# Performance work log

Measured on AMD Instinct MI355X. Metric: run time of the kernel, lower is better.

The kernel has to match this reference:

```python
import jax, jax.numpy as jnp
import numpy as np

B, P, D = 256, 128, 768        # batch, property slots per sample, encoder hidden dim
E = 64                          # num_properties (number of adapter heads)
H = 256                         # adapter_hidden_dim
H2 = H // 2
O = 2                           # output_dim
LN_EPS = 1e-5
RES_W_ADPT, RES_W_BASE = 0.7, 0.3


def setup_inputs() -> dict:
    key = jax.random.key(0)
    ks = jax.random.split(key, 12)
    hidden_states = jax.random.normal(ks[0], (B, P, D), dtype=jnp.float32)
    base_output = jax.random.normal(ks[1], (B, P, O), dtype=jnp.float32)
    properties = jax.random.randint(ks[2], (B, P), 0, E, dtype=jnp.int64)
    mask = (jax.random.uniform(ks[3], (B, P)) > 0.1).astype(jnp.float32)
    # Stacked per-head adapter parameters (LayerNorm + 3 Linears per head)
    ln_g = jnp.ones((E, D), dtype=jnp.float32)
    ln_b = jnp.zeros((E, D), dtype=jnp.float32)
    W1 = jax.random.normal(ks[4], (E, D, H), dtype=jnp.float32) * (1.0 / np.sqrt(D))
    b1 = jnp.zeros((E, H), dtype=jnp.float32)
    W2 = jax.random.normal(ks[5], (E, H, H2), dtype=jnp.float32) * (1.0 / np.sqrt(H))
    b2 = jnp.zeros((E, H2), dtype=jnp.float32)
    W3 = jax.random.normal(ks[6], (E, H2, O), dtype=jnp.float32) * 0.01  # init std=0.01 per source
    b3 = jnp.zeros((E, O), dtype=jnp.float32)
    return {
        "hidden_states": hidden_states, "base_output": base_output,
        "properties": properties, "mask": mask,
        "ln_g": ln_g, "ln_b": ln_b, "W1": W1, "b1": b1,
        "W2": W2, "b2": b2, "W3": W3, "b3": b3,
    }


def reference(hidden_states, base_output, properties, mask,
              ln_g, ln_b, W1, b1, W2, b2, W3, b3):
    b, p, d = hidden_states.shape
    o = W3.shape[-1]
    x = hidden_states.reshape(-1, d)                        # [N, D]
    # LayerNorm statistics are head-independent; only gamma/beta differ per head
    mu = jnp.mean(x, axis=-1, keepdims=True)
    var = jnp.mean((x - mu) ** 2, axis=-1, keepdims=True)
    xhat = (x - mu) * jax.lax.rsqrt(var + LN_EPS)           # [N, D]
    flat_p = properties.reshape(-1)                         # [N]
    flat_m = mask.reshape(-1)                               # [N]

    def body(acc, inp):
        idx, g, bt, w1, bb1, w2, bb2, w3, bb3 = inp
        h = jax.nn.relu((xhat * g + bt) @ w1 + bb1)         # [N, H]  (dropout = identity in eval)
        h = jax.nn.relu(h @ w2 + bb2)                       # [N, H2]
        out = h @ w3 + bb3                                  # [N, O]
        sel = (flat_p == idx) & (flat_m > 0)
        return jnp.where(sel[:, None], out, acc), None

    e = W1.shape[0]
    acc0 = jnp.zeros((b * p, o), dtype=x.dtype)
    acc, _ = jax.lax.scan(
        body, acc0,
        (jnp.arange(e), ln_g, ln_b, W1, b1, W2, b2, W3, b3))
    out = acc.reshape(b, p, o)
    out = RES_W_ADPT * out + RES_W_BASE * base_output       # use_residual=True
    return out * mask[..., None]
```

## Files before the change

kernel.cpp:

```cpp
#include <hip/hip_runtime.h>
#include <stdint.h>

typedef unsigned short u16;
typedef unsigned int   u32;

#define NTOK   32768
#define GD     768
#define GH     256
#define GH2    128
#define GE     64

typedef __bf16 bf16x8 __attribute__((ext_vector_type(8)));
typedef float  f32x4  __attribute__((ext_vector_type(4)));
union Frag { uint4 u; bf16x8 b; };

__device__ __forceinline__ float bf2f(u16 h) {
  union { u32 u; float f; } v; v.u = ((u32)h) << 16; return v.f;
}
__device__ __forceinline__ u16 f2bf(float f) {
  union { float f; u32 u; } v; v.f = f;
  u32 r = (v.u + 0x7fffu + ((v.u >> 16) & 1u)) >> 16;
  return (u16)r;
}

__device__ __forceinline__ void async16(void* lds, const void* g) {
  __builtin_amdgcn_global_load_lds(
      (const __attribute__((address_space(1))) void*)g,
      (__attribute__((address_space(3))) void*)lds, 16, 0, 0);
}

__device__ __forceinline__ int getProp(const int* p32, int t, int is64) {
  return is64 ? p32[2 * t] : p32[t];
}

static const size_t OFF_Y    = 0;
static const size_t OFF_W1T  = 50331648;
static const size_t OFF_W2T  = 75497472;
static const size_t OFF_TOK  = 79691776;
static const size_t OFF_META = 79822848;

__global__ void setup_kernel(const int* __restrict__ prop, const float* __restrict__ mask,
                             u32* __restrict__ outz, int* __restrict__ counts2d,
                             int* __restrict__ cursors_p, int* __restrict__ flagp) {
  __shared__ int h[GE];
  __shared__ int vOr;
  const int b = blockIdx.x;
  const int tid = threadIdx.x;
  outz[b * 512 + tid] = 0u;
  outz[b * 512 + 256 + tid] = 0u;
  if (b < 4) cursors_p[b * 256 + tid] = 0;
  if (tid < GE) h[tid] = 0;
  if (tid == 0) vOr = 0;
  __syncthreads();
  int v = prop[2 * tid + 1] | prop[2 * (tid + 256) + 1];
  if (v) atomicOr(&vOr, 1);
  __syncthreads();
  const int is64 = (vOr == 0) ? 1 : 0;
  if (b == 0 && tid == 0) *flagp = is64;
  const int t = b * 256 + tid;
  if (mask[t] > 0.f) atomicAdd(&h[getProp(prop, t, is64)], 1);
  __syncthreads();
  if (tid < GE) counts2d[b * GE + tid] = h[tid];
}

__global__ void transpose_w1(const float* __restrict__ in, u16* __restrict__ out) {
  __shared__ u16 tl[64][260];
  const int bid = blockIdx.x;
  const int e  = bid / 12, r = bid % 12;
  const int d0 = (r / 4) * 256, h0 = (r % 4) * 64;
  const int tid = threadIdx.x;
  const size_t inMat = (size_t)e * GD * GH;
  const size_t outMat = (size_t)e * GH * GD;
  const int h_l = (tid & 15) * 4, d_l = tid >> 4;
#pragma unroll
  for (int dd = 0; dd < 16; ++dd) {
    const int d = d_l + dd * 16;
    float4 v = *(const float4*)(in + inMat + (size_t)(d0 + d) * GH + h0 + h_l);
    tl[h_l + 0][d] = f2bf(v.x);
    tl[h_l + 1][d] = f2bf(v.y);
    tl[h_l + 2][d] = f2bf(v.z);
    tl[h_l + 3][d] = f2bf(v.w);
  }
  __syncthreads();
  const int wv = tid >> 6, ln = tid & 63;
#pragma unroll
  for (int hh = 0; hh < 16; ++hh) {
    const int h = wv * 16 + hh;
    *(uint2*)(out + outMat + (size_t)(h0 + h) * GD + d0 + ln * 4) =
        *(const uint2*)&tl[h][ln * 4];
  }
}

__global__ void transpose_kernel(const float* __restrict__ in, u16* __restrict__ out,
                                 int R, int C, int tilesC) {
  __shared__ u16 tile[32][33];
  const int tilesPerMat = (R >> 5) * tilesC;
  const int e  = blockIdx.x / tilesPerMat;
  const int t  = blockIdx.x % tilesPerMat;
  const int tr = t / tilesC, tc = t % tilesC;
  const size_t mat = (size_t)e * R * C;
  const int tx = threadIdx.x & 31, ty = threadIdx.x >> 5;
  const int r0 = tr * 32, c0 = tc * 32;
#pragma unroll
  for (int i = 0; i < 32; i += 8)
    tile[ty + i][tx] = f2bf(in[mat + (size_t)(r0 + ty + i) * C + c0 + tx]);
  __syncthreads();
#pragma unroll
  for (int i = 0; i < 32; i += 8)
    out[mat + (size_t)(c0 + ty + i) * R + r0 + tx] = tile[tx][ty + i];
}

__global__ void ln_kernel(const float* __restrict__ hs, const float* __restrict__ g,
                          const float* __restrict__ bta, const int* __restrict__ prop,
                          u16* __restrict__ y, const int* __restrict__ flag) {
  const int wv = threadIdx.x >> 6, ln = threadIdx.x & 63;
  const int t = blockIdx.x * 4 + wv;
  const float* x = hs + (size_t)t * GD;
  float v[12];
  float s = 0.f, sq = 0.f;
#pragma unroll
  for (int c = 0; c < 3; ++c) {
    float4 u = *(const float4*)(x + c * 256 + ln * 4);
    v[c*4+0] = u.x; v[c*4+1] = u.y; v[c*4+2] = u.z; v[c*4+3] = u.w;
    s  += u.x + u.y + u.z + u.w;
    sq += u.x*u.x + u.y*u.y + u.z*u.z + u.w*u.w;
  }
#pragma unroll
  for (int d = 1; d < 64; d <<= 1) { s += __shfl_xor(s, d); sq += __shfl_xor(sq, d); }
  const float mu = s * (1.f / 768.f);
  const float rstd = rsqrtf(sq * (1.f / 768.f) - mu * mu + 1e-5f);
  const int p = getProp(prop, t, *flag);
  const float* gp = g + (size_t)p * GD;
  const float* bp = bta + (size_t)p * GD;
  u16* yp = y + (size_t)t * GD;
#pragma unroll
  for (int c = 0; c < 3; ++c) {
    float4 ug = *(const float4*)(gp + c * 256 + ln * 4);
    float4 ub = *(const float4*)(bp + c * 256 + ln * 4);
    float y0 = (v[c*4+0] - mu) * rstd * ug.x + ub.x;
    float y1 = (v[c*4+1] - mu) * rstd * ug.y + ub.y;
    float y2 = (v[c*4+2] - mu) * rstd * ug.z + ub.z;
    float y3 = (v[c*4+3] - mu) * rstd * ug.w + ub.w;
    uint2 o;
    o.x = (u32)f2bf(y0) | ((u32)f2bf(y1) << 16);
    o.y = (u32)f2bf(y2) | ((u32)f2bf(y3) << 16);
    *(uint2*)(yp + c * 256 + ln * 4) = o;
  }
}

__global__ void scan_kernel(const int* __restrict__ counts2d, int* __restrict__ offsets,
                            int* __restrict__ tileHead, int* __restrict__ tileRow,
                            int* __restrict__ nTilesPtr) {
  const int e = threadIdx.x;
  int c = 0;
  for (int b = 0; b < 128; ++b) c += counts2d[b * GE + e];
  int inc = c;
#pragma unroll
  for (int d = 1; d < 64; d <<= 1) { int n = __shfl_up(inc, d); if (e >= d) inc += n; }
  const int off = inc - c;
  offsets[e] = off;
  if (e == 63) offsets[64] = inc;
  int ntile = (c + 63) >> 6;
  int inct = ntile;
#pragma unroll
  for (int d = 1; d < 64; d <<= 1) { int n = __shfl_up(inct, d); if (e >= d) inct += n; }
  const int tb = inct - ntile;
  for (int j = 0; j < ntile; ++j) { tileHead[tb + j] = e; tileRow[tb + j] = off + j * 64; }
  if (e == 63) *nTilesPtr = inct;
}

__global__ void scatter_kernel(const int* __restrict__ prop, const float* __restrict__ mask,
                               const int* __restrict__ offsets, int* __restrict__ cursors_p,
                               int* __restrict__ tokenIds, const int* __restrict__ flag) {
  __shared__ int h[GE];
  __shared__ int basebin[GE];
  const int tid = threadIdx.x;
  const int t = blockIdx.x * 256 + tid;
  if (tid < GE) h[tid] = 0;
  __syncthreads();
  int p = -1, rank = 0;
  if (mask[t] > 0.f) {
    p = getProp(prop, t, *flag);
    rank = atomicAdd(&h[p], 1);
  }
  __syncthreads();
  if (tid < GE && h[tid] > 0) basebin[tid] = atomicAdd(&cursors_p[tid * 16], h[tid]);
  __syncthreads();
  if (p >= 0) tokenIds[offsets[p] + basebin[p] + rank] = t;
}

__global__ __launch_bounds__(256, 2) void adapter_gemm(
    const u16* __restrict__ y, const u16* __restrict__ w1t, const u16* __restrict__ w2t,
    const float* __restrict__ b1, const float* __restrict__ b2,
    const float* __restrict__ w3, const float* __restrict__ b3,
    const float* __restrict__ base, const float* __restrict__ mask,
    const int* __restrict__ tokenIds, const int* __restrict__ offsets,
    const int* __restrict__ tileHead, const int* __restrict__ tileRow,
    const int* __restrict__ nTilesPtr, float* __restrict__ outp) {
  __shared__ union LU {
    struct { u16 A[2][2048]; u16 B[2][8192]; } s;
    u16 h[17408];
  } uni;
  __shared__ u16 sB2[2][4096];
  __shared__ float sBias1[256];
  __shared__ float sBias2[128];
  __shared__ float sW3[2][128];
  __shared__ float sB3[2];
  __shared__ int   sTok[64];

  const int tid  = threadIdx.x;
  const int wv   = tid >> 6;
  const int ln   = tid & 63;
  const int l15  = tid & 15;
  const int quad = (tid & 63) >> 4;
  const f32x4 vzero = {0.f, 0.f, 0.f, 0.f};
  const int nt = *nTilesPtr;

  for (int tile = blockIdx.x; tile < nt; tile += gridDim.x) {
    __syncthreads();
    const int e  = tileHead[tile];
    const int rs = tileRow[tile];
    const int nRows = min(64, offsets[e + 1] - rs);

    if (tid < 64) sTok[tid] = tokenIds[rs + min(tid, nRows - 1)];
    sBias1[tid] = b1[e * GH + tid];
    if (tid < 128) sBias2[tid] = b2[e * GH2 + tid];
    { const int k = tid >> 1, o = tid & 1; sW3[o][k] = w3[e * GH2 * 2 + k * 2 + o]; }
    if (tid < 2) sB3[tid] = b3[e * 2 + tid];
    __syncthreads();

    const u16* yrow = y + (size_t)sTok[ln] * GD;
    const u16* w1e = w1t + (size_t)e * GH * GD;
    const u16* w2e = w2t + (size_t)e * GH2 * GH;

    f32x4 acc1[4][4];
#pragma unroll
    for (int f = 0; f < 4; ++f)
#pragma unroll
      for (int g = 0; g < 4; ++g) acc1[f][g] = vzero;

    {
      async16(uni.s.A[0] + wv * 512, yrow + wv * 8);
#pragma unroll
      for (int j = 0; j < 4; ++j)
        async16(uni.s.B[0] + wv * 2048 + j * 512,
                w1e + (size_t)(j * 64 + ln) * GD + wv * 8);
    }

    for (int kt = 0; kt < 24; ++kt) {
      __syncthreads();
      if (kt + 1 < 24) {
        const int k0 = (kt + 1) * 32;
        const int par = (kt + 1) & 1;
        async16(uni.s.A[par] + wv * 512, yrow + k0 + wv * 8);
#pragma unroll
        for (int j = 0; j < 4; ++j)
          async16(uni.s.B[par] + wv * 2048 + j * 512,
                  w1e + (size_t)(j * 64 + ln) * GD + k0 + wv * 8);
      }
      const int par = kt & 1;
      Frag fa[4], fb[4];
#pragma unroll
      for (int f = 0; f < 4; ++f)
        fa[f].u = *(const uint4*)&uni.s.A[par][quad * 512 + (f * 16 + l15) * 8];
#pragma unroll
      for (int g = 0; g < 4; ++g)
        fb[g].u = *(const uint4*)&uni.s.B[par][quad * 2048 + (wv * 64 + g * 16 + l15) * 8];
#pragma unroll
      for (int f = 0; f < 4; ++f)
#pragma unroll
        for (int g = 0; g < 4; ++g)
          acc1[f][g] = __builtin_amdgcn_mfma_f32_16x16x32_bf16(fa[f].b, fb[g].b, acc1[f][g], 0, 0, 0);
    }
    __syncthreads();

#pragma unroll
    for (int j = 0; j < 2; ++j)
      async16(sB2[0] + wv * 1024 + j * 512,
              w2e + (size_t)(j * 64 + ln) * GH + wv * 8);

#pragma unroll
    for (int f = 0; f < 4; ++f)
#pragma unroll
      for (int g = 0; g < 4; ++g) {
        const int col = wv * 64 + g * 16 + l15;
        const float bias = sBias1[col];
#pragma unroll
        for (int r = 0; r < 4; ++r) {
          const int row = f * 16 + quad * 4 + r;
          uni.h[row * 264 + col] = f2bf(fmaxf(acc1[f][g][r] + bias, 0.f));
        }
      }

    f32x4 acc2[4][2];
#pragma unroll
    for (int f = 0; f < 4; ++f)
#pragma unroll
      for (int g = 0; g < 2; ++g) acc2[f][g] = vzero;

    for (int kt = 0; kt < 8; ++kt) {
      __syncthreads();
      if (kt + 1 < 8) {
        const int k0 = (kt + 1) * 32;
        const int par = (kt + 1) & 1;
#pragma unroll
        for (int j = 0; j < 2; ++j)
          async16(sB2[par] + wv * 1024 + j * 512,
                  w2e + (size_t)(j * 64 + ln) * GH + k0 + wv * 8);
      }
      const int par = kt & 1;
      Frag fa2[4], fb2[2];
#pragma unroll
      for (int f = 0; f < 4; ++f)
        fa2[f].u = *(const uint4*)&uni.h[(f * 16 + l15) * 264 + kt * 32 + quad * 8];
#pragma unroll
      for (int g = 0; g < 2; ++g)
        fb2[g].u = *(const uint4*)&sB2[par][quad * 1024 + (wv * 32 + g * 16 + l15) * 8];
#pragma unroll
      for (int f = 0; f < 4; ++f)
#pragma unroll
        for (int g = 0; g < 2; ++g)
          acc2[f][g] = __builtin_amdgcn_mfma_f32_16x16x32_bf16(fa2[f].b, fb2[g].b, acc2[f][g], 0, 0, 0);
    }
    __syncthreads();

#pragma unroll
    for (int f = 0; f < 4; ++f)
#pragma unroll
      for (int g = 0; g < 2; ++g) {
        const int col = wv * 32 + g * 16 + l15;
        const float bias = sBias2[col];
#pragma unroll
        for (int r = 0; r < 4; ++r) {
          const int row = f * 16 + quad * 4 + r;
          uni.h[row * 130 + col] = f2bf(fmaxf(acc2[f][g][r] + bias, 0.f));
        }
      }
    __syncthreads();

    const int m = tid >> 1, o = tid & 1;
    if (m < nRows) {
      float a = sB3[o];
      const u16* h2row = &uni.h[m * 130];
#pragma unroll 16
      for (int k = 0; k < 128; ++k) a += bf2f(h2row[k]) * sW3[o][k];
      const int t = sTok[m];
      const float mk = mask[t];
      const float bs = base[t * 2 + o];
      outp[t * 2 + o] = (0.7f * a + 0.3f * bs) * mk;
    }
  }
}

extern "C" void kernel_launch(void* const* d_in, const int* in_sizes, int n_in,
                              void* d_out, int out_size, void* d_ws, size_t ws_size,
                              hipStream_t stream) {
  const float* hs   = (const float*)d_in[0];
  const float* base = (const float*)d_in[1];
  const int*   prop = (const int*)d_in[2];
  const float* mask = (const float*)d_in[3];
  const float* lng  = (const float*)d_in[4];
  const float* lnb  = (const float*)d_in[5];
  const float* W1   = (const float*)d_in[6];
  const float* b1   = (const float*)d_in[7];
  const float* W2   = (const float*)d_in[8];
  const float* b2   = (const float*)d_in[9];
  const float* W3   = (const float*)d_in[10];
  const float* b3   = (const float*)d_in[11];

  char* ws = (char*)d_ws;
  u16* y    = (u16*)(ws + OFF_Y);
  u16* w1t  = (u16*)(ws + OFF_W1T);
  u16* w2t  = (u16*)(ws + OFF_W2T);
  int* tok  = (int*)(ws + OFF_TOK);
  int* meta = (int*)(ws + OFF_META);
  int* counts2d  = meta;
  int* offsets   = meta + 8192;
  int* tileHead  = meta + 8320;
  int* tileRow   = meta + 9344;
  int* nTiles    = meta + 10368;
  int* propFlag  = meta + 10369;
  int* cursors_p = meta + 10432;

  setup_kernel<<<128, 256, 0, stream>>>(prop, mask, (u32*)d_out, counts2d,
                                        cursors_p, propFlag);
  transpose_w1<<<768, 256, 0, stream>>>(W1, w1t);
  transpose_kernel<<<64 * 8 * 4, 256, 0, stream>>>(W2, w2t, GH, GH2, 4);
  ln_kernel<<<NTOK / 4, 256, 0, stream>>>(hs, lng, lnb, prop, y, propFlag);
  scan_kernel<<<1, 64, 0, stream>>>(counts2d, offsets, tileHead, tileRow, nTiles);
  scatter_kernel<<<NTOK / 256, 256, 0, stream>>>(prop, mask, offsets, cursors_p, tok, propFlag);
  adapter_gemm<<<640, 256, 0, stream>>>(y, w1t, w2t, b1, b2, W3, b3, base, mask,
                                        tok, offsets, tileHead, tileRow, nTiles,
                                        (float*)d_out);
}
```

Before: 285.5 us.

## Fuse LayerNorm into adapter GEMM A-tile staging and parallelize scan

Removes the separate LayerNorm kernel and its bf16 intermediate buffer. The GEMM now computes per-row mean and rstd from the fp32 hidden states and normalizes each A tile in registers before writing it to shared memory. This is meant to drop a full write and re-read of the normalized activations, at the cost of reading each fp32 row twice inside the GEMM and using synchronous loads instead of async copies for the A operand. The scan kernel also splits the count reduction across 256 threads.

```diff
diff --git a/kernel.cpp b/kernel.cpp
--- a/kernel.cpp
+++ b/kernel.cpp
@@ -33,11 +33,10 @@
   return is64 ? p32[2 * t] : p32[t];
 }
 
-static const size_t OFF_Y    = 0;
-static const size_t OFF_W1T  = 50331648;
-static const size_t OFF_W2T  = 75497472;
-static const size_t OFF_TOK  = 79691776;
-static const size_t OFF_META = 79822848;
+static const size_t OFF_W1T  = 0;
+static const size_t OFF_W2T  = 25165824;
+static const size_t OFF_TOK  = 29360128;
+static const size_t OFF_META = 29491200;
 
 __global__ void setup_kernel(const int* __restrict__ prop, const float* __restrict__ mask,
                              u32* __restrict__ outz, int* __restrict__ counts2d,
@@ -110,63 +109,32 @@
     out[mat + (size_t)(c0 + ty + i) * R + r0 + tx] = tile[tx][ty + i];
 }
 
-__global__ void ln_kernel(const float* __restrict__ hs, const float* __restrict__ g,
-                          const float* __restrict__ bta, const int* __restrict__ prop,
-                          u16* __restrict__ y, const int* __restrict__ flag) {
-  const int wv = threadIdx.x >> 6, ln = threadIdx.x & 63;
-  const int t = blockIdx.x * 4 + wv;
-  const float* x = hs + (size_t)t * GD;
-  float v[12];
-  float s = 0.f, sq = 0.f;
-#pragma unroll
-  for (int c = 0; c < 3; ++c) {
-    float4 u = *(const float4*)(x + c * 256 + ln * 4);
-    v[c*4+0] = u.x; v[c*4+1] = u.y; v[c*4+2] = u.z; v[c*4+3] = u.w;
-    s  += u.x + u.y + u.z + u.w;
-    sq += u.x*u.x + u.y*u.y + u.z*u.z + u.w*u.w;
-  }
-#pragma unroll
-  for (int d = 1; d < 64; d <<= 1) { s += __shfl_xor(s, d); sq += __shfl_xor(sq, d); }
-  const float mu = s * (1.f / 768.f);
-  const float rstd = rsqrtf(sq * (1.f / 768.f) - mu * mu + 1e-5f);
-  const int p = getProp(prop, t, *flag);
-  const float* gp = g + (size_t)p * GD;
-  const float* bp = bta + (size_t)p * GD;
-  u16* yp = y + (size_t)t * GD;
-#pragma unroll
-  for (int c = 0; c < 3; ++c) {
-    float4 ug = *(const float4*)(gp + c * 256 + ln * 4);
-    float4 ub = *(const float4*)(bp + c * 256 + ln * 4);
-    float y0 = (v[c*4+0] - mu) * rstd * ug.x + ub.x;
-    float y1 = (v[c*4+1] - mu) * rstd * ug.y + ub.y;
-    float y2 = (v[c*4+2] - mu) * rstd * ug.z + ub.z;
-    float y3 = (v[c*4+3] - mu) * rstd * ug.w + ub.w;
-    uint2 o;
-    o.x = (u32)f2bf(y0) | ((u32)f2bf(y1) << 16);
-    o.y = (u32)f2bf(y2) | ((u32)f2bf(y3) << 16);
-    *(uint2*)(yp + c * 256 + ln * 4) = o;
-  }
-}
-
 __global__ void scan_kernel(const int* __restrict__ counts2d, int* __restrict__ offsets,
                             int* __restrict__ tileHead, int* __restrict__ tileRow,
                             int* __restrict__ nTilesPtr) {
-  const int e = threadIdx.x;
+  __shared__ int part[4][GE];
+  const int tid = threadIdx.x;
+  const int e = tid & 63, q = tid >> 6;
   int c = 0;
-  for (int b = 0; b < 128; ++b) c += counts2d[b * GE + e];
-  int inc = c;
-#pragma unroll
-  for (int d = 1; d < 64; d <<= 1) { int n = __shfl_up(inc, d); if (e >= d) inc += n; }
-  const int off = inc - c;
-  offsets[e] = off;
-  if (e == 63) offsets[64] = inc;
-  int ntile = (c + 63) >> 6;
-  int inct = ntile;
-#pragma unroll
-  for (int d = 1; d < 64; d <<= 1) { int n = __shfl_up(inct, d); if (e >= d) inct += n; }
-  const int tb = inct - ntile;
-  for (int j = 0; j < ntile; ++j) { tileHead[tb + j] = e; tileRow[tb + j] = off + j * 64; }
-  if (e == 63) *nTilesPtr = inct;
+  for (int b = q * 32; b < q * 32 + 32; ++b) c += counts2d[b * GE + e];
+  part[q][e] = c;
+  __syncthreads();
+  if (tid < GE) {
+    const int ct = part[0][e] + part[1][e] + part[2][e] + part[3][e];
+    int inc = ct;
+#pragma unroll
+    for (int d = 1; d < 64; d <<= 1) { int n = __shfl_up(inc, d); if (e >= d) inc += n; }
+    const int off = inc - ct;
+    offsets[e] = off;
+    if (e == 63) offsets[64] = inc;
+    int ntile = (ct + 63) >> 6;
+    int inct = ntile;
+#pragma unroll
+    for (int d = 1; d < 64; d <<= 1) { int n = __shfl_up(inct, d); if (e >= d) inct += n; }
+    const int tb = inct - ntile;
+    for (int j = 0; j < ntile; ++j) { tileHead[tb + j] = e; tileRow[tb + j] = off + j * 64; }
+    if (e == 63) *nTilesPtr = inct;
+  }
 }
 
 __global__ void scatter_kernel(const int* __restrict__ prop, const float* __restrict__ mask,
@@ -190,7 +158,8 @@
 }
 
 __global__ __launch_bounds__(256, 2) void adapter_gemm(
-    const u16* __restrict__ y, const u16* __restrict__ w1t, const u16* __restrict__ w2t,
+    const float* __restrict__ hs, const u16* __restrict__ w1t, const u16* __restrict__ w2t,
+    const float* __restrict__ lng, const float* __restrict__ lnb,
     const float* __restrict__ b1, const float* __restrict__ b2,
     const float* __restrict__ w3, const float* __restrict__ b3,
     const float* __restrict__ base, const float* __restrict__ mask,
@@ -207,6 +176,10 @@
   __shared__ float sW3[2][128];
   __shared__ float sB3[2];
   __shared__ int   sTok[64];
+  __shared__ __align__(16) float sGam[GD];
+  __shared__ __align__(16) float sBet[GD];
+  __shared__ float sMu[64];
+  __shared__ float sRstd[64];
 
   const int tid  = threadIdx.x;
   const int wv   = tid >> 6;
@@ -229,34 +202,85 @@
     if (tid < 2) sB3[tid] = b3[e * 2 + tid];
     __syncthreads();
 
-    const u16* yrow = y + (size_t)sTok[ln] * GD;
     const u16* w1e = w1t + (size_t)e * GH * GD;
     const u16* w2e = w2t + (size_t)e * GH2 * GH;
 
+#pragma unroll
+    for (int j = 0; j < 4; ++j)
+      async16(uni.s.B[0] + wv * 2048 + j * 512,
+              w1e + (size_t)(j * 64 + ln) * GD + wv * 8);
+
+    if (tid < 192) {
+      *(float4*)&sGam[tid * 4] = *(const float4*)(lng + (size_t)e * GD + tid * 4);
+      *(float4*)&sBet[tid * 4] = *(const float4*)(lnb + (size_t)e * GD + tid * 4);
+    }
+
+#pragma unroll 2
+    for (int pass = 0; pass < 4; ++pass) {
+      const int row = pass * 16 + (tid >> 4);
+      const int l16 = tid & 15;
+      const float* xp = hs + (size_t)sTok[row] * GD + l16 * 4;
+      float s = 0.f, sq = 0.f;
+#pragma unroll
+      for (int c = 0; c < 12; ++c) {
+        float4 u = *(const float4*)(xp + c * 64);
+        s  += u.x + u.y + u.z + u.w;
+        sq += u.x*u.x + u.y*u.y + u.z*u.z + u.w*u.w;
+      }
+#pragma unroll
+      for (int d = 1; d < 16; d <<= 1) { s += __shfl_xor(s, d); sq += __shfl_xor(sq, d); }
+      if (l16 == 0) {
+        const float mu = s * (1.f / 768.f);
+        sMu[row] = mu;
+        sRstd[row] = rsqrtf(sq * (1.f / 768.f) - mu * mu + 1e-5f);
+      }
+    }
+    __syncthreads();
+
+    const int r0  = tid >> 3;
+    const int klo = (tid & 7) * 4;
+    const int kgrp = klo >> 3, kin = klo & 7;
+    const float* xA = hs + (size_t)sTok[r0] * GD + klo;
+    const float* xB = hs + (size_t)sTok[r0 + 32] * GD + klo;
+    const float muA = sMu[r0],      rsA = sRstd[r0];
+    const float muB = sMu[r0 + 32], rsB = sRstd[r0 + 32];
+
+#define STAGE_A(K0, PAR) do {                                                   \
+    const float4 gv = *(const float4*)&sGam[(K0) + klo];                        \
+    const float4 bv = *(const float4*)&sBet[(K0) + klo];                        \
+    float4 va = *(const float4*)(xA + (K0));                                    \
+    float4 vb = *(const float4*)(xB + (K0));                                    \
+    uint2 oa, ob;                                                               \
+    oa.x = (u32)f2bf((va.x - muA) * rsA * gv.x + bv.x)                          \
+         | ((u32)f2bf((va.y - muA) * rsA * gv.y + bv.y) << 16);                 \
+    oa.y = (u32)f2bf((va.z - muA) * rsA * gv.z + bv.z)                          \
+         | ((u32)f2bf((va.w - muA) * rsA * gv.w + bv.w) << 16);                 \
+    ob.x = (u32)f2bf((vb.x - muB) * rsB * gv.x + bv.x)                          \
+         | ((u32)f2bf((vb.y - muB) * rsB * gv.y + bv.y) << 16);                 \
+    ob.y = (u32)f2bf((vb.z - muB) * rsB * gv.z + bv.z)                          \
+         | ((u32)f2bf((vb.w - muB) * rsB * gv.w + bv.w) << 16);                 \
+    *(uint2*)&uni.s.A[PAR][kgrp * 512 + r0 * 8 + kin] = oa;                     \
+    *(uint2*)&uni.s.A[PAR][kgrp * 512 + (r0 + 32) * 8 + kin] = ob;              \
+  } while (0)
+
     f32x4 acc1[4][4];
 #pragma unroll
     for (int f = 0; f < 4; ++f)
 #pragma unroll
       for (int g = 0; g < 4; ++g) acc1[f][g] = vzero;
 
-    {
-      async16(uni.s.A[0] + wv * 512, yrow + wv * 8);
-#pragma unroll
-      for (int j = 0; j < 4; ++j)
-        async16(uni.s.B[0] + wv * 2048 + j * 512,
-                w1e + (size_t)(j * 64 + ln) * GD + wv * 8);
-    }
+    STAGE_A(0, 0);
 
     for (int kt = 0; kt < 24; ++kt) {
       __syncthreads();
       if (kt + 1 < 24) {
         const int k0 = (kt + 1) * 32;
         const int par = (kt + 1) & 1;
-        async16(uni.s.A[par] + wv * 512, yrow + k0 + wv * 8);
 #pragma unroll
         for (int j = 0; j < 4; ++j)
           async16(uni.s.B[par] + wv * 2048 + j * 512,
                   w1e + (size_t)(j * 64 + ln) * GD + k0 + wv * 8);
+        STAGE_A(k0, par);
       }
       const int par = kt & 1;
       Frag fa[4], fb[4];
@@ -350,6 +374,7 @@
       outp[t * 2 + o] = (0.7f * a + 0.3f * bs) * mk;
     }
   }
+#undef STAGE_A
 }
 
 extern "C" void kernel_launch(void* const* d_in, const int* in_sizes, int n_in,
@@ -369,7 +394,6 @@
   const float* b3   = (const float*)d_in[11];
 
   char* ws = (char*)d_ws;
-  u16* y    = (u16*)(ws + OFF_Y);
   u16* w1t  = (u16*)(ws + OFF_W1T);
   u16* w2t  = (u16*)(ws + OFF_W2T);
   int* tok  = (int*)(ws + OFF_TOK);
@@ -386,10 +410,9 @@
                                         cursors_p, propFlag);
   transpose_w1<<<768, 256, 0, stream>>>(W1, w1t);
   transpose_kernel<<<64 * 8 * 4, 256, 0, stream>>>(W2, w2t, GH, GH2, 4);
-  ln_kernel<<<NTOK / 4, 256, 0, stream>>>(hs, lng, lnb, prop, y, propFlag);
-  scan_kernel<<<1, 64, 0, stream>>>(counts2d, offsets, tileHead, tileRow, nTiles);
+  scan_kernel<<<1, 256, 0, stream>>>(counts2d, offsets, tileHead, tileRow, nTiles);
   scatter_kernel<<<NTOK / 256, 256, 0, stream>>>(prop, mask, offsets, cursors_p, tok, propFlag);
-  adapter_gemm<<<640, 256, 0, stream>>>(y, w1t, w2t, b1, b2, W3, b3, base, mask,
-                                        tok, offsets, tileHead, tileRow, nTiles,
-                                        (float*)d_out);
-}
+  adapter_gemm<<<640, 256, 0, stream>>>(hs, w1t, w2t, lng, lnb, b1, b2, W3, b3,
+                                        base, mask, tok, offsets, tileHead, tileRow,
+                                        nTiles, (float*)d_out);
+}
```

Result: faster. 276.6 us (-3.1%).
